# Kernel tuning notes

Hardware: AMD Instinct MI355X
Metric: run time of the kernel (lower is better)

The kernel has to match this reference:

```python
import jax, jax.numpy as jnp
import numpy as np

EPS = 1e-12
SIMILARITY = 'l2'


def setup_inputs() -> dict:
    key = jax.random.key(0)
    k1, k2, k3, k4 = jax.random.split(key, 4)
    N, M, D = 8192, 8192, 256
    x = jax.random.normal(k1, (N, D), dtype=jnp.float32)
    x_n = jax.random.normal(k2, (M, D), dtype=jnp.float32)
    W = jax.random.normal(k3, (D, 2), dtype=jnp.float32) / np.sqrt(D)
    b = jax.random.normal(k4, (2,), dtype=jnp.float32)
    return {"x": x, "x_n": x_n, "W": W, "b": b}


def _sim_matrix(x, x_n, similarity):
    if similarity == 'l2':
        x2 = jnp.sum(x * x, axis=1, keepdims=True)          # [N,1]
        xn2 = jnp.sum(x_n * x_n, axis=1, keepdims=True).T    # [1,M]
        d2 = jnp.maximum(x2 + xn2 - 2.0 * (x @ x_n.T), 0.0)
        return -jnp.sqrt(d2)
    elif similarity == 'l1':
        return -jnp.sum(jnp.abs(x[:, None, :] - x_n[None, :, :]), axis=-1)
    elif similarity == 'dot':
        return (x @ x_n.T) / x.shape[1]
    elif similarity == 'cos':
        xn_ = x / jnp.linalg.norm(x, axis=1, keepdims=True)
        xnn = x_n / jnp.linalg.norm(x_n, axis=1, keepdims=True)
        return xn_ @ xnn.T
    raise ValueError(similarity)


def reference(x, x_n, W, b) -> jnp.ndarray:
    # soft-KNN params from a small linear head
    params = jax.nn.sigmoid(x @ W + b)                      # [N,2]
    k = jnp.clip(params[:, 0:1], EPS, 1.0 - EPS)            # [N,1]
    t = jnp.clip(params[:, 1:2], EPS, 1.0 - EPS)            # [N,1]

    sim = _sim_matrix(x, x_n, SIMILARITY)                   # [N,M]
    sim_min = jnp.min(sim, axis=1, keepdims=True)
    sim_max = jnp.max(sim, axis=1, keepdims=True)
    sim = (sim - sim_min) / (sim_max - sim_min)             # row min-max normalize
    sim = jnp.maximum(sim, EPS)

    shift = t / (1.0 - t) * (k - sim) * jnp.log(sim / k)
    return sim + jnp.where(sim <= k, shift, 0.0)
```

## Files before the change

### kernel.cpp

```cpp
#include <hip/hip_runtime.h>
#include <hip/hip_bf16.h>
#include <cstdint>

#define N_ROWS 8192
#define M_ROWS 8192
#define DDIM   256
#define EPSF   1e-12f

typedef unsigned short u16;
typedef __attribute__((ext_vector_type(8))) short short8;
typedef __attribute__((ext_vector_type(4))) float floatx4;

__device__ inline void split_bf16(float v, u16& h, u16& lo) {
    __hip_bfloat16 hb = __float2bfloat16(v);
    float hf = __bfloat162float(hb);
    __hip_bfloat16 lb = __float2bfloat16(v - hf);
    h  = __builtin_bit_cast(u16, hb);
    lo = __builtin_bit_cast(u16, lb);
}

__global__ __launch_bounds__(256) void prep_x(
    const float* __restrict__ x, const float* __restrict__ W, const float* __restrict__ b,
    u16* __restrict__ xhi, u16* __restrict__ xlo,
    float* __restrict__ x2, float* __restrict__ karr, float* __restrict__ Carr,
    float* __restrict__ logkarr)
{
    const int l = threadIdx.x & 63;
    const int w = threadIdx.x >> 6;
    const int row = blockIdx.x * 4 + w;

    const float4 xv = *(const float4*)(x + (size_t)row * DDIM + l * 4);
    const float4 wa = *(const float4*)(W + l * 8);
    const float4 wb = *(const float4*)(W + l * 8 + 4);

    float s2 = xv.x * xv.x + xv.y * xv.y + xv.z * xv.z + xv.w * xv.w;
    float s0 = xv.x * wa.x + xv.y * wa.z + xv.z * wb.x + xv.w * wb.z;
    float s1 = xv.x * wa.y + xv.y * wa.w + xv.z * wb.y + xv.w * wb.w;

    u16 h0, l0, h1, l1, h2, l2, h3, l3;
    split_bf16(xv.x, h0, l0); split_bf16(xv.y, h1, l1);
    split_bf16(xv.z, h2, l2); split_bf16(xv.w, h3, l3);
    *(ushort4*)(xhi + (size_t)row * DDIM + l * 4) = make_ushort4(h0, h1, h2, h3);
    *(ushort4*)(xlo + (size_t)row * DDIM + l * 4) = make_ushort4(l0, l1, l2, l3);

    #pragma unroll
    for (int off = 32; off; off >>= 1) {
        s2 += __shfl_xor(s2, off);
        s0 += __shfl_xor(s0, off);
        s1 += __shfl_xor(s1, off);
    }
    if (l == 0) {
        float a0 = s0 + b[0];
        float a1 = s1 + b[1];
        float k = 1.0f / (1.0f + __expf(-a0));
        float t = 1.0f / (1.0f + __expf(-a1));
        k = fminf(fmaxf(k, EPSF), 1.0f - EPSF);
        t = fminf(fmaxf(t, EPSF), 1.0f - EPSF);
        x2[row] = s2;
        karr[row] = k;
        Carr[row] = t / (1.0f - t);
        logkarr[row] = logf(k);
    }
}

__global__ __launch_bounds__(256) void prep_xn(
    const float* __restrict__ xn,
    u16* __restrict__ xnhi, u16* __restrict__ xnlo, float* __restrict__ xn2)
{
    const int l = threadIdx.x & 63;
    const int w = threadIdx.x >> 6;
    const int row = blockIdx.x * 4 + w;

    const float4 xv = *(const float4*)(xn + (size_t)row * DDIM + l * 4);
    float s2 = xv.x * xv.x + xv.y * xv.y + xv.z * xv.z + xv.w * xv.w;

    u16 h0, l0, h1, l1, h2, l2, h3, l3;
    split_bf16(xv.x, h0, l0); split_bf16(xv.y, h1, l1);
    split_bf16(xv.z, h2, l2); split_bf16(xv.w, h3, l3);
    *(ushort4*)(xnhi + (size_t)row * DDIM + l * 4) = make_ushort4(h0, h1, h2, h3);
    *(ushort4*)(xnlo + (size_t)row * DDIM + l * 4) = make_ushort4(l0, l1, l2, l3);

    #pragma unroll
    for (int off = 32; off; off >>= 1) s2 += __shfl_xor(s2, off);
    if (l == 0) xn2[row] = s2;
}

__global__ __launch_bounds__(512, 2) void gemm_s(
    const u16* __restrict__ xhi, const u16* __restrict__ xlo,
    const u16* __restrict__ xnhi, const u16* __restrict__ xnlo,
    const float* __restrict__ x2, const float* __restrict__ xn2,
    float* __restrict__ out)
{
    extern __shared__ char lds[];

    const int tid = threadIdx.x;
    const int l   = tid & 63;
    const int w   = tid >> 6;
    const int wm  = w >> 2;
    const int wn  = w & 3;

    const int wg   = blockIdx.x;
    const int swz  = (wg & 7) * 128 + (wg >> 3);
    const int bRow = swz >> 5;
    const int bCol = swz & 31;

    const int srow = tid >> 3;
    const int scol = (((tid & 7) ^ ((tid >> 3) & 7)) << 3);
    const size_t aSrc = (size_t)(bRow * 256 + srow) * DDIM + scol;
    const size_t bSrc = (size_t)(bCol * 256 + srow) * DDIM + scol;

#define STAGE(T, BUF) do {                                                        \
    const u16* pa_ = ((T) < 8) ? xhi : xlo;                                       \
    const u16* pb_ = (((T) >> 2) == 1) ? xnlo : xnhi;                             \
    const int  ko_ = ((T) & 3) * 64;                                              \
    char* da_ = lds + (BUF) * 65536;                                              \
    char* db_ = da_ + 32768;                                                      \
    _Pragma("unroll")                                                             \
    for (int j_ = 0; j_ < 4; ++j_) {                                              \
        __builtin_amdgcn_global_load_lds(                                         \
            (const __attribute__((address_space(1))) void*)(pa_ + aSrc + (size_t)j_ * 16384 + ko_), \
            (__attribute__((address_space(3))) void*)(da_ + j_ * 8192 + tid * 16), 16, 0, 0); \
        __builtin_amdgcn_global_load_lds(                                         \
            (const __attribute__((address_space(1))) void*)(pb_ + bSrc + (size_t)j_ * 16384 + ko_), \
            (__attribute__((address_space(3))) void*)(db_ + j_ * 8192 + tid * 16), 16, 0, 0); \
    } } while (0)

    floatx4 acc[8][4];
    #pragma unroll
    for (int mi = 0; mi < 8; ++mi)
        #pragma unroll
        for (int ni = 0; ni < 4; ++ni)
            acc[mi][ni] = (floatx4){0.f, 0.f, 0.f, 0.f};

    const int laneRow = l & 15;
    const int laneKb  = (l >> 4) << 4;
    const int laneSwz = (l & 7) << 4;
    const int aRowB = (wm * 128 + laneRow) * 128;
    const int bRowB = (wn * 64  + laneRow) * 128;

    STAGE(0, 0);
    STAGE(1, 1);

    for (int t = 0; t < 12; ++t) {
        if (t < 11) asm volatile("s_waitcnt vmcnt(8)" ::: "memory");
        else        asm volatile("s_waitcnt vmcnt(0)" ::: "memory");
        __builtin_amdgcn_s_barrier();

        const char* pA = lds + (t & 1) * 65536;
        const char* pB = pA + 32768;

        #pragma unroll
        for (int ks = 0; ks < 2; ++ks) {
            const int kb = (ks * 64 + laneKb) ^ laneSwz;
            short8 ah[8], bh[4];
            #pragma unroll
            for (int mi = 0; mi < 8; ++mi)
                ah[mi] = *(const short8*)(pA + aRowB + mi * 2048 + kb);
            #pragma unroll
            for (int ni = 0; ni < 4; ++ni)
                bh[ni] = *(const short8*)(pB + bRowB + ni * 2048 + kb);
            asm volatile("s_waitcnt lgkmcnt(0)" ::: "memory");
            __builtin_amdgcn_sched_barrier(0);
            __builtin_amdgcn_s_setprio(1);
            #pragma unroll
            for (int mi = 0; mi < 8; ++mi)
                #pragma unroll
                for (int ni = 0; ni < 4; ++ni)
                    acc[mi][ni] = __builtin_amdgcn_mfma_f32_16x16x32_bf16(ah[mi], bh[ni], acc[mi][ni], 0, 0, 0);
            __builtin_amdgcn_s_setprio(0);
            __builtin_amdgcn_sched_barrier(0);
            if (ks == 0) __builtin_amdgcn_s_barrier();
        }
        __builtin_amdgcn_s_barrier();
        if (t + 2 < 12) STAGE(t + 2, t & 1);
    }
#undef STAGE

    const int q  = l >> 4;
    const int cn = l & 15;
    const int rowBase = bRow * 256 + wm * 128;
    const int colBase = bCol * 256 + wn * 64;
    #pragma unroll
    for (int mi = 0; mi < 8; ++mi) {
        #pragma unroll
        for (int r = 0; r < 4; ++r) {
            const int i = rowBase + mi * 16 + q * 4 + r;
            const float x2i = x2[i];
            #pragma unroll
            for (int ni = 0; ni < 4; ++ni) {
                const int j = colBase + ni * 16 + cn;
                const float d2 = x2i + xn2[j] - 2.0f * acc[mi][ni][r];
                out[(size_t)i * M_ROWS + j] = -sqrtf(fmaxf(d2, 0.0f));
            }
        }
    }
}

__global__ __launch_bounds__(256) void transform_row(
    float* __restrict__ out, const float* __restrict__ x, const float* __restrict__ xn,
    const float* __restrict__ karr, const float* __restrict__ Carr,
    const float* __restrict__ logkarr)
{
    const int row = blockIdx.x;
    const int t = threadIdx.x;
    const int l = t & 63;
    const int w = t >> 6;

    __shared__ float wmin[4], wmax[4];
    __shared__ int cnt;
    __shared__ unsigned long long sMinBits;
    __shared__ int cidx[1024];
    __shared__ double cval[1024];

    const size_t rbase = (size_t)row * M_ROWS;
    float4 v[8];
    #pragma unroll
    for (int c = 0; c < 8; ++c)
        v[c] = *(const float4*)(out + rbase + c * 1024 + t * 4);

    float lmin = 1e30f, lmax = -1e30f;
    #pragma unroll
    for (int c = 0; c < 8; ++c) {
        lmin = fminf(lmin, fminf(fminf(v[c].x, v[c].y), fminf(v[c].z, v[c].w)));
        lmax = fmaxf(lmax, fmaxf(fmaxf(v[c].x, v[c].y), fmaxf(v[c].z, v[c].w)));
    }
    #pragma unroll
    for (int m = 1; m < 64; m <<= 1) {
        lmin = fminf(lmin, __shfl_xor(lmin, m));
        lmax = fmaxf(lmax, __shfl_xor(lmax, m));
    }
    if (l == 0) { wmin[w] = lmin; wmax[w] = lmax; }
    if (t == 0) { cnt = 0; sMinBits = 0ull; }
    __syncthreads();
    const float sminA = fminf(fminf(wmin[0], wmin[1]), fminf(wmin[2], wmin[3]));
    const float smaxA = fmaxf(fmaxf(wmax[0], wmax[1]), fmaxf(wmax[2], wmax[3]));
    const float thresh = sminA + 0.05f * (smaxA - sminA);

    int myPos[8], mySlot[8];
    int myCnt = 0;
    #pragma unroll
    for (int c = 0; c < 8; ++c) {
        const float* pv = (const float*)&v[c];
        #pragma unroll
        for (int u = 0; u < 4; ++u) {
            if (pv[u] <= thresh) {
                int pos = atomicAdd(&cnt, 1);
                if (pos < 1024 && myCnt < 8) {
                    cidx[pos] = c * 1024 + t * 4 + u;
                    myPos[myCnt] = pos;
                    mySlot[myCnt] = c * 4 + u;
                    myCnt++;
                }
            }
        }
    }
    __syncthreads();
    const int nc = min(cnt, 1024);

    const float4 xa = *(const float4*)(x + (size_t)row * DDIM + l * 4);
    const double dx0 = xa.x, dx1 = xa.y, dx2 = xa.z, dx3 = xa.w;
    double x2p = dx0 * dx0 + dx1 * dx1 + dx2 * dx2 + dx3 * dx3;
    #pragma unroll
    for (int m = 1; m < 64; m <<= 1) x2p += __shfl_xor(x2p, m);

    for (int c = w; c < nc; c += 4) {
        const int j = cidx[c];
        const float4 na = *(const float4*)(xn + (size_t)j * DDIM + l * 4);
        const double n0 = na.x, n1 = na.y, n2 = na.z, n3 = na.w;
        double dot = dx0 * n0 + dx1 * n1 + dx2 * n2 + dx3 * n3;
        double nn  = n0 * n0 + n1 * n1 + n2 * n2 + n3 * n3;
        #pragma unroll
        for (int m = 1; m < 64; m <<= 1) {
            dot += __shfl_xor(dot, m);
            nn  += __shfl_xor(nn, m);
        }
        if (l == 0) {
            double d2 = x2p + nn - 2.0 * dot;
            d2 = d2 > 0.0 ? d2 : 0.0;
            double se = -sqrt(d2);
            cval[c] = se;
            atomicMax(&sMinBits, (unsigned long long)__double_as_longlong(se));
        }
    }
    __syncthreads();

    const double sminD = __longlong_as_double((long long)sMinBits);
    const float k = karr[row], C = Carr[row], logk = logkarr[row];
    const float smin = (float)sminD;
    const double invD = 1.0 / ((double)smaxA - sminD);
    const float inv = (float)invD;

    float o[32];
    #pragma unroll
    for (int c = 0; c < 8; ++c) {
        const float* pv = (const float*)&v[c];
        #pragma unroll
        for (int u = 0; u < 4; ++u) {
            float sim = fmaxf((pv[u] - smin) * inv, EPSF);
            float r = sim;
            if (sim <= k) r += C * (k - sim) * (__logf(sim) - logk);
            o[c * 4 + u] = r;
        }
    }
    for (int q2 = 0; q2 < myCnt; ++q2) {
        double simd = (cval[myPos[q2]] - sminD) * invD;
        simd = simd > (double)EPSF ? simd : (double)EPSF;
        float sim = (float)simd;
        float r = sim;
        if (sim <= k) r += C * (k - sim) * (logf(sim) - logk);
        o[mySlot[q2]] = r;
    }
    #pragma unroll
    for (int c = 0; c < 8; ++c) {
        float4 ov;
        ov.x = o[c * 4 + 0]; ov.y = o[c * 4 + 1];
        ov.z = o[c * 4 + 2]; ov.w = o[c * 4 + 3];
        *(float4*)(out + rbase + c * 1024 + t * 4) = ov;
    }
}

extern "C" void kernel_launch(void* const* d_in, const int* in_sizes, int n_in,
                              void* d_out, int out_size, void* d_ws, size_t ws_size,
                              hipStream_t stream)
{
    const float* x  = (const float*)d_in[0];
    const float* xn = (const float*)d_in[1];
    const float* W  = (const float*)d_in[2];
    const float* b  = (const float*)d_in[3];
    float* out = (float*)d_out;

    uint8_t* ws = (uint8_t*)d_ws;
    u16* xhi  = (u16*)(ws);
    u16* xlo  = (u16*)(ws + (4u << 20));
    u16* xnhi = (u16*)(ws + (8u << 20));
    u16* xnlo = (u16*)(ws + (12u << 20));
    float* x2       = (float*)(ws + (16u << 20));
    float* xn2      = x2 + N_ROWS;
    float* karr     = xn2 + M_ROWS;
    float* Carr     = karr + N_ROWS;
    float* logkarr  = Carr + N_ROWS;

    static bool attr_done = false;
    if (!attr_done) {
        (void)hipFuncSetAttribute(reinterpret_cast<const void*>(gemm_s),
                                  hipFuncAttributeMaxDynamicSharedMemorySize, 131072);
        attr_done = true;
    }

    prep_x<<<N_ROWS / 4, 256, 0, stream>>>(x, W, b, xhi, xlo, x2, karr, Carr, logkarr);
    prep_xn<<<M_ROWS / 4, 256, 0, stream>>>(xn, xnhi, xnlo, xn2);
    gemm_s<<<1024, 512, 131072, stream>>>(xhi, xlo, xnhi, xnlo, x2, xn2, out);
    transform_row<<<N_ROWS, 256, 0, stream>>>(out, x, xn, karr, Carr, logkarr);
}
```

Before: 475.3 us.

## Split GEMM main loop into four quadrant phases with interleaved LDS staging

```diff
diff --git a/kernel.cpp b/kernel.cpp
--- a/kernel.cpp
+++ b/kernel.cpp
@@ -99,31 +99,44 @@
     const int wm  = w >> 2;
     const int wn  = w & 3;
 
-    const int wg   = blockIdx.x;
-    const int swz  = (wg & 7) * 128 + (wg >> 3);
-    const int bRow = swz >> 5;
-    const int bCol = swz & 31;
+    const int wg    = blockIdx.x;
+    const int xcd   = wg & 7;
+    const int seq   = wg >> 3;
+    const int rnd   = seq >> 5;
+    const int idx   = seq & 31;
+    const int cell  = rnd * 8 + xcd;
+    const int rg    = cell & 7;
+    const int cg    = cell >> 3;
+    const int bRow  = rg * 4 + (idx & 3);
+    const int bCol  = cg * 8 + (idx >> 2);
 
     const int srow = tid >> 3;
-    const int scol = (((tid & 7) ^ ((tid >> 3) & 7)) << 3);
-    const size_t aSrc = (size_t)(bRow * 256 + srow) * DDIM + scol;
-    const size_t bSrc = (size_t)(bCol * 256 + srow) * DDIM + scol;
-
-#define STAGE(T, BUF) do {                                                        \
-    const u16* pa_ = ((T) < 8) ? xhi : xlo;                                       \
-    const u16* pb_ = (((T) >> 2) == 1) ? xnlo : xnhi;                             \
-    const int  ko_ = ((T) & 3) * 64;                                              \
-    char* da_ = lds + (BUF) * 65536;                                              \
-    char* db_ = da_ + 32768;                                                      \
-    _Pragma("unroll")                                                             \
-    for (int j_ = 0; j_ < 4; ++j_) {                                              \
-        __builtin_amdgcn_global_load_lds(                                         \
-            (const __attribute__((address_space(1))) void*)(pa_ + aSrc + (size_t)j_ * 16384 + ko_), \
-            (__attribute__((address_space(3))) void*)(da_ + j_ * 8192 + tid * 16), 16, 0, 0); \
-        __builtin_amdgcn_global_load_lds(                                         \
-            (const __attribute__((address_space(1))) void*)(pb_ + bSrc + (size_t)j_ * 16384 + ko_), \
-            (__attribute__((address_space(3))) void*)(db_ + j_ * 8192 + tid * 16), 16, 0, 0); \
-    } } while (0)
+    const int scol = (((tid & 7) ^ (srow & 7)) << 3);
+    const int dcol = (tid & 7) * 16;
+    const int rA1_0 = srow,               rA1_1 = srow + 128;
+    const int rA2_0 = srow + 64,          rA2_1 = srow + 192;
+    const int rB1_0 = srow + (srow & 32), rB1_1 = rB1_0 + 128;
+    const int rB2_0 = rB1_0 + 32,         rB2_1 = rB1_0 + 160;
+    const size_t aG = (size_t)bRow * 256;
+    const size_t bG = (size_t)bCol * 256;
+
+#define APAN(T) (((T) < 8) ? xhi : xlo)
+#define BPAN(T) ((((T) >> 2) == 1) ? xnlo : xnhi)
+#define KOFF(T) (((T) & 3) * 64)
+#define LDSA(T) (lds + ((T) & 1) * 65536)
+#define LDSB(T) (lds + ((T) & 1) * 65536 + 32768)
+#define SU(pan, gbase, ldsbase, r0, r1, ko) do {                                  \
+    __builtin_amdgcn_global_load_lds(                                             \
+        (const __attribute__((address_space(1))) void*)((pan) + ((gbase) + (r0)) * (size_t)DDIM + (ko) + scol), \
+        (__attribute__((address_space(3))) void*)((ldsbase) + (r0) * 128 + dcol), 16, 0, 0); \
+    __builtin_amdgcn_global_load_lds(                                             \
+        (const __attribute__((address_space(1))) void*)((pan) + ((gbase) + (r1)) * (size_t)DDIM + (ko) + scol), \
+        (__attribute__((address_space(3))) void*)((ldsbase) + (r1) * 128 + dcol), 16, 0, 0); \
+} while (0)
+#define SU_A1(T) SU(APAN(T), aG, LDSA(T), rA1_0, rA1_1, KOFF(T))
+#define SU_A2(T) SU(APAN(T), aG, LDSA(T), rA2_0, rA2_1, KOFF(T))
+#define SU_B1(T) SU(BPAN(T), bG, LDSB(T), rB1_0, rB1_1, KOFF(T))
+#define SU_B2(T) SU(BPAN(T), bG, LDSB(T), rB2_0, rB2_1, KOFF(T))
 
     floatx4 acc[8][4];
     #pragma unroll
@@ -137,44 +150,112 @@
     const int laneSwz = (l & 7) << 4;
     const int aRowB = (wm * 128 + laneRow) * 128;
     const int bRowB = (wn * 64  + laneRow) * 128;
-
-    STAGE(0, 0);
-    STAGE(1, 1);
+    const int kb0 = laneKb ^ laneSwz;
+    const int kb1 = (64 + laneKb) ^ laneSwz;
+
+    SU_A1(0); SU_B1(0); SU_B2(0); SU_A2(0);
+    SU_B1(1); SU_A1(1); SU_B2(1);
+
+    short8 a[4][2], b01[2][2], b23[2][2];
 
     for (int t = 0; t < 12; ++t) {
-        if (t < 11) asm volatile("s_waitcnt vmcnt(8)" ::: "memory");
+        const char* pA = LDSA(t);
+        const char* pB = LDSB(t);
+
+        if (t < 11) asm volatile("s_waitcnt vmcnt(6)" ::: "memory");
         else        asm volatile("s_waitcnt vmcnt(0)" ::: "memory");
-        __builtin_amdgcn_s_barrier();
-
-        const char* pA = lds + (t & 1) * 65536;
-        const char* pB = pA + 32768;
-
-        #pragma unroll
-        for (int ks = 0; ks < 2; ++ks) {
-            const int kb = (ks * 64 + laneKb) ^ laneSwz;
-            short8 ah[8], bh[4];
+        if (t + 1 < 12) SU_A2(t + 1);
+        __builtin_amdgcn_s_barrier();
+        #pragma unroll
+        for (int mi = 0; mi < 4; ++mi) {
+            a[mi][0] = *(const short8*)(pA + aRowB + mi * 2048 + kb0);
+            a[mi][1] = *(const short8*)(pA + aRowB + mi * 2048 + kb1);
+        }
+        #pragma unroll
+        for (int ni = 0; ni < 2; ++ni) {
+            b01[ni][0] = *(const short8*)(pB + bRowB + ni * 2048 + kb0);
+            b01[ni][1] = *(const short8*)(pB + bRowB + ni * 2048 + kb1);
+        }
+        asm volatile("s_waitcnt lgkmcnt(0)" ::: "memory");
+        __builtin_amdgcn_sched_barrier(0);
+        __builtin_amdgcn_s_setprio(1);
+        #pragma unroll
+        for (int mi = 0; mi < 4; ++mi)
             #pragma unroll
-            for (int mi = 0; mi < 8; ++mi)
-                ah[mi] = *(const short8*)(pA + aRowB + mi * 2048 + kb);
+            for (int ni = 0; ni < 2; ++ni) {
+                acc[mi][ni] = __builtin_amdgcn_mfma_f32_16x16x32_bf16(a[mi][0], b01[ni][0], acc[mi][ni], 0, 0, 0);
+                acc[mi][ni] = __builtin_amdgcn_mfma_f32_16x16x32_bf16(a[mi][1], b01[ni][1], acc[mi][ni], 0, 0, 0);
+            }
+        __builtin_amdgcn_s_setprio(0);
+        __builtin_amdgcn_sched_barrier(0);
+        __builtin_amdgcn_s_barrier();
+
+        if (t + 2 < 12) SU_B1(t + 2);
+        #pragma unroll
+        for (int ni = 0; ni < 2; ++ni) {
+            b23[ni][0] = *(const short8*)(pB + bRowB + (2 + ni) * 2048 + kb0);
+            b23[ni][1] = *(const short8*)(pB + bRowB + (2 + ni) * 2048 + kb1);
+        }
+        __builtin_amdgcn_s_barrier();
+        asm volatile("s_waitcnt lgkmcnt(0)" ::: "memory");
+        __builtin_amdgcn_sched_barrier(0);
+        __builtin_amdgcn_s_setprio(1);
+        #pragma unroll
+        for (int mi = 0; mi < 4; ++mi)
             #pragma unroll
-            for (int ni = 0; ni < 4; ++ni)
-                bh[ni] = *(const short8*)(pB + bRowB + ni * 2048 + kb);
-            asm volatile("s_waitcnt lgkmcnt(0)" ::: "memory");
-            __builtin_amdgcn_sched_barrier(0);
-            __builtin_amdgcn_s_setprio(1);
+            for (int ni = 0; ni < 2; ++ni) {
+                acc[mi][2 + ni] = __builtin_amdgcn_mfma_f32_16x16x32_bf16(a[mi][0], b23[ni][0], acc[mi][2 + ni], 0, 0, 0);
+                acc[mi][2 + ni] = __builtin_amdgcn_mfma_f32_16x16x32_bf16(a[mi][1], b23[ni][1], acc[mi][2 + ni], 0, 0, 0);
+            }
+        __builtin_amdgcn_s_setprio(0);
+        __builtin_amdgcn_sched_barrier(0);
+        __builtin_amdgcn_s_barrier();
+
+        if (t + 2 < 12) SU_A1(t + 2);
+        #pragma unroll
+        for (int mi = 0; mi < 4; ++mi) {
+            a[mi][0] = *(const short8*)(pA + aRowB + (4 + mi) * 2048 + kb0);
+            a[mi][1] = *(const short8*)(pA + aRowB + (4 + mi) * 2048 + kb1);
+        }
+        __builtin_amdgcn_s_barrier();
+        asm volatile("s_waitcnt lgkmcnt(0)" ::: "memory");
+        __builtin_amdgcn_sched_barrier(0);
+        __builtin_amdgcn_s_setprio(1);
+        #pragma unroll
+        for (int mi = 0; mi < 4; ++mi)
             #pragma unroll
-            for (int mi = 0; mi < 8; ++mi)
-                #pragma unroll
-                for (int ni = 0; ni < 4; ++ni)
-                    acc[mi][ni] = __builtin_amdgcn_mfma_f32_16x16x32_bf16(ah[mi], bh[ni], acc[mi][ni], 0, 0, 0);
-            __builtin_amdgcn_s_setprio(0);
-            __builtin_amdgcn_sched_barrier(0);
-            if (ks == 0) __builtin_amdgcn_s_barrier();
-        }
-        __builtin_amdgcn_s_barrier();
-        if (t + 2 < 12) STAGE(t + 2, t & 1);
-    }
-#undef STAGE
+            for (int ni = 0; ni < 2; ++ni) {
+                acc[4 + mi][ni] = __builtin_amdgcn_mfma_f32_16x16x32_bf16(a[mi][0], b01[ni][0], acc[4 + mi][ni], 0, 0, 0);
+                acc[4 + mi][ni] = __builtin_amdgcn_mfma_f32_16x16x32_bf16(a[mi][1], b01[ni][1], acc[4 + mi][ni], 0, 0, 0);
+            }
+        __builtin_amdgcn_s_setprio(0);
+        __builtin_amdgcn_sched_barrier(0);
+        __builtin_amdgcn_s_barrier();
+
+        if (t + 2 < 12) SU_B2(t + 2);
+        __builtin_amdgcn_s_barrier();
+        __builtin_amdgcn_s_setprio(1);
+        #pragma unroll
+        for (int mi = 0; mi < 4; ++mi)
+            #pragma unroll
+            for (int ni = 0; ni < 2; ++ni) {
+                acc[4 + mi][2 + ni] = __builtin_amdgcn_mfma_f32_16x16x32_bf16(a[mi][0], b23[ni][0], acc[4 + mi][2 + ni], 0, 0, 0);
+                acc[4 + mi][2 + ni] = __builtin_amdgcn_mfma_f32_16x16x32_bf16(a[mi][1], b23[ni][1], acc[4 + mi][2 + ni], 0, 0, 0);
+            }
+        __builtin_amdgcn_s_setprio(0);
+        __builtin_amdgcn_sched_barrier(0);
+        __builtin_amdgcn_s_barrier();
+    }
+#undef SU_A1
+#undef SU_A2
+#undef SU_B1
+#undef SU_B2
+#undef SU
+#undef APAN
+#undef BPAN
+#undef KOFF
+#undef LDSA
+#undef LDSB
 
     const int q  = l >> 4;
     const int cn = l & 15;
```

Result: no change. 472.1 us (-0.7%).
